# Optimization experiments

Measured on AMD Instinct MI355X. Metric: run time of the kernel, lower is better.

Reference implementation:

```python
import jax, jax.numpy as jnp
import numpy as np

ALPHA = 0.1
MAX_ITER = 35
TOL = 0.01
STEP = ALPHA / 2.0  # step_size = alpha/2 as in TV2DFunction.forward


def _prox_tv1d(step, y):
    """Exact 1D TV prox via taut-string lower/upper hulls (faithful port of _prox_tv1d)."""
    n = y.shape[0]
    width = n + 1
    dt = y.dtype
    cs = jnp.cumsum(y)
    y_low = jnp.concatenate([jnp.zeros(1, dt), cs - step]).at[width - 1].add(step)
    y_up = jnp.concatenate([jnp.zeros(1, dt), cs + step]).at[width - 1].add(-step)

    inf = jnp.asarray(jnp.inf, dt)
    il = jnp.zeros(width, jnp.int32)   # index_low
    iu = jnp.zeros(width, jnp.int32)   # index_up
    idx = jnp.zeros(width, jnp.int32)  # breakpoint indices
    sl = jnp.zeros(width, dt).at[0].set(inf)    # slope_low
    su = jnp.zeros(width, dt).at[0].set(-inf)   # slope_up
    z = jnp.zeros(width, dt)
    zero = jnp.int32(0)

    def fdiv(num, a, b):
        # a > b always holds on the taken branch; maximum() only guards the
        # unselected jnp.where branch against NaN/Inf.
        return num / jnp.maximum(a - b, 1).astype(dt)

    def body(i, st):
        il, sl, iu, su, idx, z, s_l, c_l, s_u, c_u, c = st
        c_l = c_l + 1
        c_u = c_u + 1
        il = il.at[c_l].set(i)
        iu = iu.at[c_u].set(i)
        sl = sl.at[c_l].set(y_low[i] - y_low[i - 1])

        def w1_cond(t):
            il_, sl_, c_l_ = t
            return (c_l_ > s_l + 1) & (sl_[jnp.maximum(s_l, c_l_ - 1)] <= sl_[c_l_])

        def w1_body(t):
            il_, sl_, c_l_ = t
            c_l_ = c_l_ - 1
            il_ = il_.at[c_l_].set(i)
            ns = jnp.where(c_l_ > s_l + 1,
                           fdiv(y_low[i] - y_low[il_[c_l_ - 1]], i, il_[c_l_ - 1]),
                           fdiv(y_low[i] - z[c], i, idx[c]))
            return il_, sl_.at[c_l_].set(ns), c_l_

        il, sl, c_l = jax.lax.while_loop(w1_cond, w1_body, (il, sl, c_l))

        su = su.at[c_u].set(y_up[i] - y_up[i - 1])

        def w2_cond(t):
            iu_, su_, c_u_ = t
            return (c_u_ > s_u + 1) & (su_[jnp.maximum(s_u, c_u_ - 1)] >= su_[c_u_])

        def w2_body(t):
            iu_, su_, c_u_ = t
            c_u_ = c_u_ - 1
            iu_ = iu_.at[c_u_].set(i)
            ns = jnp.where(c_u_ > s_u + 1,
                           fdiv(y_up[i] - y_up[iu_[c_u_ - 1]], i, iu_[c_u_ - 1]),
                           fdiv(y_up[i] - z[c], i, idx[c]))
            return iu_, su_.at[c_u_].set(ns), c_u_

        iu, su, c_u = jax.lax.while_loop(w2_cond, w2_body, (iu, su, c_u))

        def w3_cond(t):
            idx_, z_, sl_, il_, s_u_, c_ = t
            return (c_l == s_l + 1) & (c_u > s_u_ + 1) & (sl_[c_l] >= su[s_u_ + 1])

        def w3_body(t):
            idx_, z_, sl_, il_, s_u_, c_ = t
            c_ = c_ + 1
            s_u_ = s_u_ + 1
            k = iu[s_u_]
            idx_ = idx_.at[c_].set(k)
            z_ = z_.at[c_].set(y_up[k])
            il_ = il_.at[s_l].set(k)
            sl_ = sl_.at[c_l].set(fdiv(y_low[i] - y_up[k], i, k))
            return idx_, z_, sl_, il_, s_u_, c_

        idx, z, sl, il, s_u, c = jax.lax.while_loop(w3_cond, w3_body, (idx, z, sl, il, s_u, c))

        def w4_cond(t):
            idx_, z_, su_, iu_, s_l_, c_ = t
            return (c_u == s_u + 1) & (c_l > s_l_ + 1) & (su_[c_u] <= sl[s_l_ + 1])

        def w4_body(t):
            idx_, z_, su_, iu_, s_l_, c_ = t
            c_ = c_ + 1
            s_l_ = s_l_ + 1
            k = il[s_l_]
            idx_ = idx_.at[c_].set(k)
            z_ = z_.at[c_].set(y_low[k])
            iu_ = iu_.at[s_u].set(k)
            su_ = su_.at[c_u].set(fdiv(y_up[i] - y_low[k], i, k))
            return idx_, z_, su_, iu_, s_l_, c_

        idx, z, su, iu, s_l, c = jax.lax.while_loop(w4_cond, w4_body, (idx, z, su, iu, s_l, c))

        return il, sl, iu, su, idx, z, s_l, c_l, s_u, c_u, c

    st = (il, sl, iu, su, idx, z, zero, zero, zero, zero, zero)
    il, sl, iu, su, idx, z, s_l, c_l, s_u, c_u, c = jax.lax.fori_loop(1, width, body, st)

    # tail: append remaining lower-hull points to the breakpoint list
    m = c_l - s_l
    offs = jnp.arange(width)
    valid = (offs >= 1) & (offs <= m)
    src = il[jnp.clip(s_l + offs, 0, width - 1)]
    tgt = jnp.where(valid, c + offs, width)  # 'width' is out of bounds -> dropped
    idx = idx.at[tgt].set(src, mode='drop')
    z = z.at[tgt].set(y_low[src], mode='drop')
    c = c + m

    # piecewise-constant output: slope of taut string on each segment
    a = (z - jnp.roll(z, 1)) / jnp.maximum(idx - jnp.roll(idx, 1), 1).astype(dt)
    knots = jnp.where(offs <= c, idx, n + 1)  # sorted; idx[c] == n
    seg = jnp.searchsorted(knots, jnp.arange(n), side='right')  # segment id in [1, c]
    return a[seg]


def _prox_cols(step, A):
    return jax.vmap(lambda col: _prox_tv1d(step, col), in_axes=1, out_axes=1)(A)


def _prox_rows(step, A):
    return jax.vmap(lambda row: _prox_tv1d(step, row))(A)


def _prox_tv2d(x, step, max_iter, tol):
    """Douglas-Rachford splitting for 2D TV prox (Barbero & Sra 2014)."""
    def cond(carry):
        it, x_, p, q, acc = carry
        return (it < max_iter) & (acc >= tol)

    def body(carry):
        it, x_, p, q, _ = carry
        y = _prox_cols(step, x_ + p)
        p = p + x_ - y
        x2 = _prox_rows(step, y + q)
        q = q + y - x2
        acc = jnp.max(jnp.abs(y - x2))
        return it + 1, x2, p, q, acc

    z0 = jnp.zeros_like(x)
    init = (jnp.int32(0), x, z0, z0, jnp.asarray(jnp.inf, x.dtype))
    return jax.lax.while_loop(cond, body, init)[1]


def setup_inputs() -> dict:
    key = jax.random.key(0)
    X = jax.random.normal(key, (256, 256), dtype=jnp.float32)
    return {"X": X}


def reference(X):
    return _prox_tv2d(X, STEP, MAX_ITER, TOL)
```

## Files before the change

kernel.cpp:

```cpp
#include <hip/hip_runtime.h>

#define N 256
#define NLINE 4
#define NB (N / NLINE)
#define NT (NLINE * 64)
#define LAM 0.05f
#define TWOLAM (2.0f * LAM)
#define FOURLAM (4.0f * LAM)
#define MAXIT 35
#define TOL 0.01f

__device__ __forceinline__ float rlane(float v, int lane) {
    return __int_as_float(__builtin_amdgcn_readlane(__float_as_int(v), lane));
}

struct Dist { float r0, r1, r2, r3; };

__device__ __forceinline__ float dfetch(const Dist& d, int k) {
    const int lane = k & 63;
    const int sel = k >> 6;
    float a = rlane(d.r0, lane);
    float b = rlane(d.r1, lane);
    float c = rlane(d.r2, lane);
    float e = rlane(d.r3, lane);
    float ab = (sel & 1) ? b : a;
    float ce = (sel & 1) ? e : c;
    return (sel & 2) ? ce : ab;
}

__device__ __forceinline__ void flushseg(Dist& o, int lo, int hi, float val, int lane) {
    const unsigned len = (unsigned)(hi - lo);
    const int base = lane - lo;
    o.r0 = ((unsigned)(base      ) <= len) ? val : o.r0;
    o.r1 = ((unsigned)(base + 64 ) <= len) ? val : o.r1;
    o.r2 = ((unsigned)(base + 128) <= len) ? val : o.r2;
    o.r3 = ((unsigned)(base + 192) <= len) ? val : o.r3;
}

__device__ __forceinline__ unsigned long long sel4(unsigned long long a, unsigned long long b,
                                                   unsigned long long c, unsigned long long d, int r) {
    unsigned long long ab = (r & 1) ? b : a;
    unsigned long long cd = (r & 1) ? d : c;
    return (r & 2) ? cd : ab;
}

__device__ void tv1d_scan(const Dist& v, Dist& o, const int lane)
{
    const float lam = LAM, mlam = -LAM, twolam = TWOLAM;

    Dist vnx;
    {
        float a0 = __shfl_down(v.r0, 1), a1 = __shfl_down(v.r1, 1);
        float a2 = __shfl_down(v.r2, 1), a3 = __shfl_down(v.r3, 1);
        const bool hi = (lane == 63);
        vnx.r0 = hi ? rlane(v.r1, 0) : a0;
        vnx.r1 = hi ? rlane(v.r2, 0) : a1;
        vnx.r2 = hi ? rlane(v.r3, 0) : a2;
        vnx.r3 = hi ? v.r3 : a3;
    }
    Dist d;
    d.r0 = vnx.r0 - v.r0;  d.r1 = vnx.r1 - v.r1;
    d.r2 = vnx.r2 - v.r2;  d.r3 = vnx.r3 - v.r3;
    const unsigned lambits = __float_as_uint(lam);
    Dist sl;
    sl.r0 = __uint_as_float((__float_as_uint(d.r0) & 0x80000000u) | lambits);
    sl.r1 = __uint_as_float((__float_as_uint(d.r1) & 0x80000000u) | lambits);
    sl.r2 = __uint_as_float((__float_as_uint(d.r2) & 0x80000000u) | lambits);
    sl.r3 = __uint_as_float((__float_as_uint(d.r3) & 0x80000000u) | lambits);
    Dist slp;
    {
        float b0 = __shfl_up(sl.r0, 1), b1 = __shfl_up(sl.r1, 1);
        float b2 = __shfl_up(sl.r2, 1), b3 = __shfl_up(sl.r3, 1);
        const bool lo = (lane == 0);
        slp.r0 = lo ? 0.0f : b0;
        slp.r1 = lo ? rlane(sl.r0, 63) : b1;
        slp.r2 = lo ? rlane(sl.r1, 63) : b2;
        slp.r3 = lo ? rlane(sl.r2, 63) : b3;
    }
    Dist e, g;
    {
        float t0 = v.r0 - slp.r0, t1 = v.r1 - slp.r1, t2 = v.r2 - slp.r2, t3 = v.r3 - slp.r3;
        e.r0 = t0 + sl.r0;  e.r1 = t1 + sl.r1;  e.r2 = t2 + sl.r2;  e.r3 = t3 + sl.r3;
        g.r0 = t0 - lam;    g.r1 = t1 - lam;    g.r2 = t2 - lam;    g.r3 = t3 - lam;
    }
    const unsigned long long S0 = __ballot(d.r0 < 0.0f);
    const unsigned long long S1 = __ballot(d.r1 < 0.0f);
    const unsigned long long S2 = __ballot(d.r2 < 0.0f);
    const unsigned long long S3 = __ballot(d.r3 < 0.0f);
    const unsigned long long B20 = __ballot(fabsf(d.r0) > TWOLAM);
    const unsigned long long B21 = __ballot(fabsf(d.r1) > TWOLAM);
    const unsigned long long B22 = __ballot(fabsf(d.r2) > TWOLAM);
    const unsigned long long B23 = __ballot(fabsf(d.r3) > TWOLAM);
    const unsigned long long B40 = __ballot(fabsf(d.r0) > FOURLAM);
    const unsigned long long B41 = __ballot(fabsf(d.r1) > FOURLAM);
    const unsigned long long B42 = __ballot(fabsf(d.r2) > FOURLAM);
    const unsigned long long B43 = __ballot(fabsf(d.r3) > FOURLAM);
    const unsigned long long Sp0 = (S0 << 1);
    const unsigned long long Sp1 = (S1 << 1) | (S0 >> 63);
    const unsigned long long Sp2 = (S2 << 1) | (S1 >> 63);
    const unsigned long long Sp3 = (S3 << 1) | (S2 >> 63);
    const unsigned long long NF0 = ~(B40 | (B20 & ~(S0 ^ Sp0)));
    const unsigned long long NF1 = ~(B41 | (B21 & ~(S1 ^ Sp1)));
    const unsigned long long NF2 = ~(B42 | (B22 & ~(S2 ^ Sp2)));
    const unsigned long long NF3 = ~((B43 | (B23 & ~(S3 ^ Sp3))) & 0x7FFFFFFFFFFFFFFFull);
    const unsigned long long FNn0 = (S0 & B20) | (~S0 & B40);
    const unsigned long long FNn1 = (S1 & B21) | (~S1 & B41);
    const unsigned long long FNn2 = (S2 & B22) | (~S2 & B42);
    const unsigned long long FNn3 = (S3 & B23) | (~S3 & B43);
    const unsigned long long FNp0 = (~S0 & B20) | (S0 & B40);
    const unsigned long long FNp1 = (~S1 & B21) | (S1 & B41);
    const unsigned long long FNp2 = (~S2 & B22) | (S2 & B42);
    const unsigned long long FNp3 = (~S3 & B23) | (S3 & B43);
    const int initFF = (int)(B40 & 1ull);

    auto firstnf = [&](int jmin) -> int {
        const int w = jmin >> 6;
        unsigned long long m = sel4(NF0, NF1, NF2, NF3, w) >> (jmin & 63);
        if (m) return jmin + (int)__builtin_ctzll(m);
        unsigned long long m1 = (w < 1) ? NF1 : 0ull;
        unsigned long long m2 = (w < 2) ? NF2 : 0ull;
        if (m1) return 64 + (int)__builtin_ctzll(m1);
        if (m2) return 128 + (int)__builtin_ctzll(m2);
        return 192 + (int)__builtin_ctzll(NF3);
    };

    auto trigbit = [&](int kk, int neg) -> int {
        const int w = kk >> 6;
        const unsigned long long m = neg ? sel4(FNn0, FNn1, FNn2, FNn3, w)
                                         : sel4(FNp0, FNp1, FNp2, FNp3, w);
        return (int)((m >> (kk & 63)) & 1ull);
    };

    int k = 0, k0 = 0, km = 0, kp = 0;
    float umin = lam, umax = mlam;
    const float v0 = rlane(v.r0, 0);
    float vmin = v0 - lam, vmax = v0 + lam;
    float flen = 1.0f;
    float rnext = 0.5f;
    float vn1 = rlane(vnx.r0, 0);
    int guard = 0;

    auto fastfwd = [&]() {
        const int K1 = firstnf(k + 1);
        const int sneg = (int)((sel4(S0, S1, S2, S3, k >> 6) >> (k & 63)) & 1ull);
        flushseg(o, k, k, sneg ? vmin : vmax, lane);
        if (K1 > k + 1) {
            const int lo = k + 1;
            const unsigned len = (unsigned)(K1 - 1 - lo);
            const int base = lane - lo;
            o.r0 = ((unsigned)(base      ) <= len) ? e.r0 : o.r0;
            o.r1 = ((unsigned)(base + 64 ) <= len) ? e.r1 : o.r1;
            o.r2 = ((unsigned)(base + 128) <= len) ? e.r2 : o.r2;
            o.r3 = ((unsigned)(base + 192) <= len) ? e.r3 : o.r3;
        }
        k = K1; k0 = K1; km = K1; kp = K1;
        vmin = dfetch(g, K1);
        vmax = vmin + twolam;
        umin = lam; umax = mlam;
        flen = 1.0f; rnext = 0.5f;
        vn1 = dfetch(vnx, K1);
    };

    auto do_step = [&]() {
        const float un = umin + vn1 - vmin;
        const float ux = umax + vn1 - vmax;
        const bool neg = un < mlam;
        const bool pos = ux > lam;
        const int wn = (k + 1) >> 6, bn = (k + 1) & 63;
        const int tn = (int)((sel4(FNn0, FNn1, FNn2, FNn3, wn) >> bn) & 1ull);
        const int tp = (int)((sel4(FNp0, FNp1, FNp2, FNp3, wn) >> bn) & 1ull);
        if (__builtin_expect((int)(neg | pos), 1)) {
            const float fval = neg ? vmin : vmax;
            const int   fhi  = neg ? km : kp;
            flushseg(o, k0, fhi, fval, lane);
            const int k0n = fhi + 1;
            float vstar;
            int trig;
            if (__builtin_expect((int)(k0n <= k), 0)) {
                vstar = dfetch(v, k0n);
                trig = trigbit(k0n, (int)neg);
            } else {
                vstar = vn1;
                trig = neg ? tn : tp;
            }
            k = k0n; k0 = k0n; km = k0n; kp = k0n;
            vmin = neg ? vstar : vstar - twolam;
            vmax = vmin + twolam;
            umin = lam; umax = mlam;
            flen = 1.0f; rnext = 0.5f;
            if (k < N - 1 && trig) {
                fastfwd();
            } else {
                vn1 = dfetch(vnx, k);
            }
        } else {
            k++;
            const float r = rnext;
            flen += 1.0f;
            const bool cmin = (un >= lam);
            const bool cmax = (ux <= mlam);
            vmin = cmin ? fmaf(un - lam, r, vmin) : vmin;
            km   = cmin ? k : km;
            umin = cmin ? lam : un;
            vmax = cmax ? fmaf(ux + lam, r, vmax) : vmax;
            kp   = cmax ? k : kp;
            umax = cmax ? mlam : ux;
            vn1 = dfetch(vnx, k);
            rnext = __builtin_amdgcn_rcpf(flen + 1.0f);
        }
    };

    if (initFF) fastfwd();

    for (;;) {
        while (k < N - 1) {
            if (++guard > 2000) return;
            do_step();
            if (k >= N - 1) break;
            do_step();
        }
        for (;;) {
            if (++guard > 4000) return;
            if (umin < 0.0f) {
                flushseg(o, k0, km, vmin, lane);
                k0 = km + 1;
                if (k0 > N - 1) return;
                km = k = k0;
                vmin = dfetch(v, k0);
                umin = lam;
                umax = vmin + lam - vmax;
                flen = 1.0f;
            } else if (umax > 0.0f) {
                flushseg(o, k0, kp, vmax, lane);
                k0 = kp + 1;
                if (k0 > N - 1) return;
                kp = k = k0;
                vmax = dfetch(v, k0);
                umax = mlam;
                umin = vmax - lam - vmin;
                flen = 1.0f;
            } else {
                vmin += umin / flen;
                flushseg(o, k0, k, vmin, lane);
                return;
            }
            if (k != N - 1) break;
        }
        rnext = 0.5f;
        vn1 = dfetch(vnx, k);
    }
}

__device__ __forceinline__ void gridbar(unsigned* flags, unsigned seq, int t) {
    __syncthreads();
    __builtin_amdgcn_fence(__ATOMIC_RELEASE, "agent");
    if (t == 0)
        __hip_atomic_store(&flags[blockIdx.x], seq, __ATOMIC_RELAXED, __HIP_MEMORY_SCOPE_AGENT);
    if (t < 64) {
        for (;;) {
            unsigned f = __hip_atomic_load(&flags[t], __ATOMIC_RELAXED, __HIP_MEMORY_SCOPE_AGENT);
            if (__all((int)(f >= seq))) break;
        }
    }
    __builtin_amdgcn_fence(__ATOMIC_ACQUIRE, "agent");
    __syncthreads();
}

__global__ __launch_bounds__(NT) void tv2d_coop(const float* __restrict__ X,
                                                float* __restrict__ xw,
                                                float* __restrict__ y,
                                                unsigned* __restrict__ flags,
                                                unsigned* __restrict__ bm)
{
    const int t = threadIdx.x;
    const int lane = t & 63;
    const int wave = t >> 6;
    const int line = blockIdx.x * NLINE + wave;
    const int col4 = 4 * blockIdx.x;
    __shared__ float tile[N * 5];
    __shared__ unsigned s_acc;
    __shared__ int s_dec;
    if (t == 0) s_acc = 0u;

    Dist p = {0.f, 0.f, 0.f, 0.f};
    Dist q = {0.f, 0.f, 0.f, 0.f};

    for (int it = 0; it < MAXIT; ++it) {
        const float* xs = (it == 0) ? X : xw;
        const float4 xc = *(const float4*)(xs + t * N + col4);
        if (it > 0) {
            if (t < 64) {
                unsigned m = __hip_atomic_load(&bm[t], __ATOMIC_RELAXED, __HIP_MEMORY_SCOPE_AGENT);
                #pragma unroll
                for (int off = 32; off > 0; off >>= 1) {
                    unsigned mm = __shfl_xor(m, off);
                    m = (mm > m) ? mm : m;
                }
                if (t == 0) s_dec = (__uint_as_float(m) < TOL) ? 1 : 0;
            }
            __syncthreads();
            if (s_dec) break;
        }
        tile[t * 5 + 0] = xc.x;
        tile[t * 5 + 1] = xc.y;
        tile[t * 5 + 2] = xc.z;
        tile[t * 5 + 3] = xc.w;
        __syncthreads();
        Dist v, o;
        v.r0 = tile[(lane      ) * 5 + wave] + p.r0;
        v.r1 = tile[(lane + 64 ) * 5 + wave] + p.r1;
        v.r2 = tile[(lane + 128) * 5 + wave] + p.r2;
        v.r3 = tile[(lane + 192) * 5 + wave] + p.r3;
        tv1d_scan(v, o, lane);
        p.r0 = v.r0 - o.r0;  p.r1 = v.r1 - o.r1;
        p.r2 = v.r2 - o.r2;  p.r3 = v.r3 - o.r3;
        float* yt = y + line * N;
        yt[lane      ] = o.r0;
        yt[lane + 64 ] = o.r1;
        yt[lane + 128] = o.r2;
        yt[lane + 192] = o.r3;
        gridbar(flags, 2u * (unsigned)it + 1u, t);

        const float4 yc = *(const float4*)(y + t * N + col4);
        tile[t * 5 + 0] = yc.x;
        tile[t * 5 + 1] = yc.y;
        tile[t * 5 + 2] = yc.z;
        tile[t * 5 + 3] = yc.w;
        __syncthreads();
        float y0 = tile[(lane      ) * 5 + wave];
        float y1 = tile[(lane + 64 ) * 5 + wave];
        float y2 = tile[(lane + 128) * 5 + wave];
        float y3 = tile[(lane + 192) * 5 + wave];
        Dist w, o2;
        w.r0 = y0 + q.r0;
        w.r1 = y1 + q.r1;
        w.r2 = y2 + q.r2;
        w.r3 = y3 + q.r3;
        tv1d_scan(w, o2, lane);
        float d0 = y0 - o2.r0;
        float d1 = y1 - o2.r1;
        float d2 = y2 - o2.r2;
        float d3 = y3 - o2.r3;
        q.r0 = w.r0 - o2.r0;  q.r1 = w.r1 - o2.r1;
        q.r2 = w.r2 - o2.r2;  q.r3 = w.r3 - o2.r3;
        float* xr = xw + line * N;
        xr[lane      ] = o2.r0;
        xr[lane + 64 ] = o2.r1;
        xr[lane + 128] = o2.r2;
        xr[lane + 192] = o2.r3;

        float am = fmaxf(fmaxf(fabsf(d0), fabsf(d1)), fmaxf(fabsf(d2), fabsf(d3)));
        #pragma unroll
        for (int off = 32; off > 0; off >>= 1)
            am = fmaxf(am, __shfl_xor(am, off));
        if (lane == 0) atomicMax(&s_acc, __float_as_uint(am));

        __syncthreads();
        if (t == 0) {
            __hip_atomic_store(&bm[blockIdx.x], s_acc, __ATOMIC_RELAXED, __HIP_MEMORY_SCOPE_AGENT);
            s_acc = 0u;
        }
        gridbar(flags, 2u * (unsigned)it + 2u, t);
    }
}

extern "C" void kernel_launch(void* const* d_in, const int* in_sizes, int n_in,
                              void* d_out, int out_size, void* d_ws, size_t ws_size,
                              hipStream_t stream) {
    const float* X = (const float*)d_in[0];
    float* xw = (float*)d_out;
    float* y = (float*)d_ws;
    unsigned* flags = (unsigned*)((char*)d_ws + (size_t)N * N * sizeof(float));
    unsigned* bm = flags + 64;
    (void)hipMemsetAsync((void*)flags, 0, NB * sizeof(unsigned), stream);
    void* args[] = { (void*)&X, (void*)&xw, (void*)&y, (void*)&flags, (void*)&bm };
    (void)hipLaunchCooperativeKernel((void*)tv2d_coop, dim3(NB), dim3(NT), args, 0, stream);
}
```

Before: 319.0 us.

## Piggyback convergence max onto grid barrier flags in padded 64-bit slots

Packs each block's convergence max into the upper half of a 64-bit barrier flag, so the barrier spin-wait also gathers the global max. This removes the separate bm array and the extra atomic loads and block sync at the top of each iteration. Slots are padded to separate 128-byte lines to reduce false sharing while spinning, and the last iteration skips the final barrier. Keeping the packed accfill in gridbar1 stops the acc half from being overwritten with stale data.

After: 304.7 us. 1.05x faster.

```diff
diff --git a/kernel.cpp b/kernel.cpp
--- a/kernel.cpp
+++ b/kernel.cpp
@@ -9,6 +9,7 @@
 #define FOURLAM (4.0f * LAM)
 #define MAXIT 35
 #define TOL 0.01f
+#define SLOTSTRIDE 16
 
 __device__ __forceinline__ float rlane(float v, int lane) {
     return __int_as_float(__builtin_amdgcn_readlane(__float_as_int(v), lane));
@@ -251,16 +252,47 @@
     }
 }
 
-__device__ __forceinline__ void gridbar(unsigned* flags, unsigned seq, int t) {
+__device__ __forceinline__ void gridbar1(unsigned long long* slots, unsigned seq,
+                                         unsigned accfill, int t) {
     __syncthreads();
     __builtin_amdgcn_fence(__ATOMIC_RELEASE, "agent");
     if (t == 0)
-        __hip_atomic_store(&flags[blockIdx.x], seq, __ATOMIC_RELAXED, __HIP_MEMORY_SCOPE_AGENT);
+        __hip_atomic_store(&slots[blockIdx.x * SLOTSTRIDE],
+                           ((unsigned long long)accfill << 32) | (unsigned long long)seq,
+                           __ATOMIC_RELAXED, __HIP_MEMORY_SCOPE_AGENT);
     if (t < 64) {
         for (;;) {
-            unsigned f = __hip_atomic_load(&flags[t], __ATOMIC_RELAXED, __HIP_MEMORY_SCOPE_AGENT);
-            if (__all((int)(f >= seq))) break;
-        }
+            unsigned long long f = __hip_atomic_load(&slots[t * SLOTSTRIDE],
+                                                     __ATOMIC_RELAXED, __HIP_MEMORY_SCOPE_AGENT);
+            if (__all((int)((unsigned)f >= seq))) break;
+        }
+    }
+    __builtin_amdgcn_fence(__ATOMIC_ACQUIRE, "agent");
+    __syncthreads();
+}
+
+__device__ __forceinline__ void gridbar2(unsigned long long* slots, unsigned seq,
+                                         unsigned acc, int t, int* s_dec) {
+    __syncthreads();
+    __builtin_amdgcn_fence(__ATOMIC_RELEASE, "agent");
+    if (t == 0)
+        __hip_atomic_store(&slots[blockIdx.x * SLOTSTRIDE],
+                           ((unsigned long long)acc << 32) | (unsigned long long)seq,
+                           __ATOMIC_RELAXED, __HIP_MEMORY_SCOPE_AGENT);
+    if (t < 64) {
+        unsigned long long f;
+        for (;;) {
+            f = __hip_atomic_load(&slots[t * SLOTSTRIDE],
+                                  __ATOMIC_RELAXED, __HIP_MEMORY_SCOPE_AGENT);
+            if (__all((int)((unsigned)f >= seq))) break;
+        }
+        unsigned a = (unsigned)(f >> 32);
+        #pragma unroll
+        for (int off = 32; off > 0; off >>= 1) {
+            unsigned aa = __shfl_xor(a, off);
+            a = (aa > a) ? aa : a;
+        }
+        if (t == 0) *s_dec = (__uint_as_float(a) < TOL) ? 1 : 0;
     }
     __builtin_amdgcn_fence(__ATOMIC_ACQUIRE, "agent");
     __syncthreads();
@@ -269,8 +301,7 @@
 __global__ __launch_bounds__(NT) void tv2d_coop(const float* __restrict__ X,
                                                 float* __restrict__ xw,
                                                 float* __restrict__ y,
-                                                unsigned* __restrict__ flags,
-                                                unsigned* __restrict__ bm)
+                                                unsigned long long* __restrict__ slots)
 {
     const int t = threadIdx.x;
     const int lane = t & 63;
@@ -284,23 +315,11 @@
 
     Dist p = {0.f, 0.f, 0.f, 0.f};
     Dist q = {0.f, 0.f, 0.f, 0.f};
+    unsigned accprev = 0u;
 
     for (int it = 0; it < MAXIT; ++it) {
         const float* xs = (it == 0) ? X : xw;
         const float4 xc = *(const float4*)(xs + t * N + col4);
-        if (it > 0) {
-            if (t < 64) {
-                unsigned m = __hip_atomic_load(&bm[t], __ATOMIC_RELAXED, __HIP_MEMORY_SCOPE_AGENT);
-                #pragma unroll
-                for (int off = 32; off > 0; off >>= 1) {
-                    unsigned mm = __shfl_xor(m, off);
-                    m = (mm > m) ? mm : m;
-                }
-                if (t == 0) s_dec = (__uint_as_float(m) < TOL) ? 1 : 0;
-            }
-            __syncthreads();
-            if (s_dec) break;
-        }
         tile[t * 5 + 0] = xc.x;
         tile[t * 5 + 1] = xc.y;
         tile[t * 5 + 2] = xc.z;
@@ -319,7 +338,7 @@
         yt[lane + 64 ] = o.r1;
         yt[lane + 128] = o.r2;
         yt[lane + 192] = o.r3;
-        gridbar(flags, 2u * (unsigned)it + 1u, t);
+        gridbar1(slots, 2u * (unsigned)it + 1u, accprev, t);
 
         const float4 yc = *(const float4*)(y + t * N + col4);
         tile[t * 5 + 0] = yc.x;
@@ -354,13 +373,15 @@
         for (int off = 32; off > 0; off >>= 1)
             am = fmaxf(am, __shfl_xor(am, off));
         if (lane == 0) atomicMax(&s_acc, __float_as_uint(am));
-
         __syncthreads();
-        if (t == 0) {
-            __hip_atomic_store(&bm[blockIdx.x], s_acc, __ATOMIC_RELAXED, __HIP_MEMORY_SCOPE_AGENT);
-            s_acc = 0u;
-        }
-        gridbar(flags, 2u * (unsigned)it + 2u, t);
+        const unsigned ba = s_acc;
+
+        if (it == MAXIT - 1) break;
+
+        gridbar2(slots, 2u * (unsigned)it + 2u, ba, t, &s_dec);
+        if (t == 0) s_acc = 0u;
+        if (s_dec) break;
+        accprev = ba;
     }
 }
 
@@ -370,9 +391,8 @@
     const float* X = (const float*)d_in[0];
     float* xw = (float*)d_out;
     float* y = (float*)d_ws;
-    unsigned* flags = (unsigned*)((char*)d_ws + (size_t)N * N * sizeof(float));
-    unsigned* bm = flags + 64;
-    (void)hipMemsetAsync((void*)flags, 0, NB * sizeof(unsigned), stream);
-    void* args[] = { (void*)&X, (void*)&xw, (void*)&y, (void*)&flags, (void*)&bm };
+    unsigned long long* slots = (unsigned long long*)((char*)d_ws + (size_t)N * N * sizeof(float));
+    (void)hipMemsetAsync((void*)slots, 0, NB * SLOTSTRIDE * sizeof(unsigned long long), stream);
+    void* args[] = { (void*)&X, (void*)&xw, (void*)&y, (void*)&slots };
     (void)hipLaunchCooperativeKernel((void*)tv2d_coop, dim3(NB), dim3(NT), args, 0, stream);
 }
```
